# Performance work log

Hardware: AMD Instinct MI355X
Metric: run time of the kernel (lower is better)

The kernel has to match this reference:

```python
import jax, jax.numpy as jnp
import numpy as np

SEQ, B, D = 2048, 16, 1024  # seq_len, batch, input/hidden size

def setup_inputs() -> dict:
    key = jax.random.key(0)
    k1, k2, k3 = jax.random.split(key, 3)
    X = jax.random.normal(k1, (SEQ, B, D), dtype=jnp.float32)
    hidden = jnp.zeros((B, D), dtype=jnp.float32)  # initial hidden state C_0
    # nn.Linear(window*input_size, 3*hidden_size): weight (3D, D), bias (3D,)
    W = jax.random.normal(k2, (3 * D, D), dtype=jnp.float32) / np.float32(np.sqrt(D))
    b = jax.random.normal(k3, (3 * D,), dtype=jnp.float32) * 0.01
    return {"X": X, "hidden": hidden, "W": W, "b": b}

def _forget_mult(F, Z, h0):
    # C_t = F_t * Z_t + (1 - F_t) * C_{t-1}, scanned over seq dim
    def step(h, fz):
        f, z = fz
        h = f * z + (1.0 - f) * h
        return h, h
    _, C = jax.lax.scan(step, h0, (F, Z))
    return C  # (S, B, D)

def reference(X, hidden, W, b):
    # window=1 -> source = X; gate projection
    Y = jnp.einsum('sbd,hd->sbh', X, W) + b        # (S, B, 3D)
    Z, F, O = jnp.split(Y, 3, axis=2)
    Z = jnp.tanh(Z)
    F = jax.nn.sigmoid(F)
    C = _forget_mult(F, Z, hidden)                 # (S, B, D)
    H = jax.nn.sigmoid(O) * C                      # output gate (QRNN-fo)
    return H, C[-1:]                               # (S,B,D), (1,B,D)
```

## Files before the change

kernel.cpp:

```cpp
#include <hip/hip_runtime.h>


#define S_LEN 2048
#define BATCH 16
#define DHID 1024
#define N3 3072
#define MROWS (S_LEN * BATCH)
#define XELEMS ((size_t)MROWS * DHID)
#define WELEMS ((size_t)N3 * DHID)
#define YELEMS ((size_t)MROWS * N3)

typedef __attribute__((ext_vector_type(8))) short bf16x8;
typedef __attribute__((ext_vector_type(4))) float floatx4;
typedef __attribute__((ext_vector_type(4))) unsigned short u16x4;

__device__ __forceinline__ float b2f(unsigned short u) {
  return __uint_as_float(((unsigned)u) << 16);
}
__device__ __forceinline__ unsigned short f2b(float x) {
  unsigned u = __float_as_uint(x);
  u += 0x7fffu + ((u >> 16) & 1u);
  return (unsigned short)(u >> 16);
}
__device__ __forceinline__ float sigmoid_f(float x) {
  return __builtin_amdgcn_rcpf(1.0f + __expf(-x));
}
__device__ __forceinline__ float tanh_f(float x) {
  return 2.0f * __builtin_amdgcn_rcpf(1.0f + __expf(-2.0f * x)) - 1.0f;
}

__device__ __forceinline__ void load_lds16(const unsigned short* g, unsigned short* l) {
  __builtin_amdgcn_global_load_lds(
      (const __attribute__((address_space(1))) void*)g,
      (__attribute__((address_space(3))) void*)l,
      16, 0, 0);
}

__global__ __launch_bounds__(256) void cvt_f32_bf16(
    const float* __restrict__ src, unsigned short* __restrict__ dst, int n4) {
  int i = blockIdx.x * 256 + threadIdx.x;
  if (i < n4) {
    float4 v = ((const float4*)src)[i];
    u16x4 o;
    o.x = f2b(v.x); o.y = f2b(v.y); o.z = f2b(v.z); o.w = f2b(v.w);
    ((u16x4*)dst)[i] = o;
  }
}

__global__ __launch_bounds__(256) void qrnn_gemm(
    const unsigned short* __restrict__ X,
    const unsigned short* __restrict__ W,
    const float* __restrict__ bias,
    unsigned short* __restrict__ Y)
{
  __shared__ __align__(16) unsigned short sA[128 * 64];
  __shared__ __align__(16) unsigned short sB[128 * 64];

  const int tid = threadIdx.x;
  const int w  = tid >> 6;
  const int l  = tid & 63;
  const int lr = l & 15;
  const int lq = l >> 4;
  const int n0B = blockIdx.x * 128;
  const int m0B = blockIdx.y * 128;
  const int wm = (w >> 1) * 64;
  const int wn = (w & 1) * 64;

  floatx4 acc[4][4] = {};

  const unsigned short* gA = X + (size_t)m0B * DHID;
  const unsigned short* gB = W + (size_t)n0B * DHID;
  const int srow = tid >> 3;
  const int scol = (tid & 7) << 3;

  for (int k0 = 0; k0 < DHID; k0 += 64) {
#pragma unroll
    for (int j = 0; j < 4; ++j) {
      load_lds16(gA + (size_t)(j * 32 + srow) * DHID + (k0 + scol),
                 sA + (j * 2048 + w * 512));
      load_lds16(gB + (size_t)(j * 32 + srow) * DHID + (k0 + scol),
                 sB + (j * 2048 + w * 512));
    }
    __syncthreads();

#pragma unroll
    for (int kk = 0; kk < 64; kk += 32) {
      bf16x8 af[4], bf[4];
#pragma unroll
      for (int i = 0; i < 4; ++i) {
        af[i] = *(const bf16x8*)&sA[(wm + i * 16 + lr) * 64 + kk + lq * 8];
      }
#pragma unroll
      for (int j = 0; j < 4; ++j) {
        bf[j] = *(const bf16x8*)&sB[(wn + j * 16 + lr) * 64 + kk + lq * 8];
      }
#pragma unroll
      for (int i = 0; i < 4; ++i) {
#pragma unroll
        for (int j = 0; j < 4; ++j) {
          acc[i][j] = __builtin_amdgcn_mfma_f32_16x16x32_bf16(
              af[i], bf[j], acc[i][j], 0, 0, 0);
        }
      }
    }
    __syncthreads();
  }

  const int seg = n0B >> 10;
#pragma unroll
  for (int j = 0; j < 4; ++j) {
    const int n = n0B + wn + j * 16 + lr;
    const float bv = bias[n];
#pragma unroll
    for (int i = 0; i < 4; ++i) {
      const int mb = m0B + wm + i * 16 + lq * 4;
#pragma unroll
      for (int r = 0; r < 4; ++r) {
        float v = acc[i][j][r] + bv;
        v = (seg == 0) ? tanh_f(v) : sigmoid_f(v);
        Y[(size_t)(mb + r) * N3 + n] = f2b(v);
      }
    }
  }
}

#define U 8
#define NCH (S_LEN / U)
#define SSTRIDE (BATCH * N3)
#define HSTRIDE (BATCH * DHID)

__global__ __launch_bounds__(64) void qrnn_scan(
    const unsigned short* __restrict__ Y,
    const float* __restrict__ h0,
    float* __restrict__ out)
{
  const int t = blockIdx.x * 64 + threadIdx.x;
  const int b = t >> 10;
  const int d = t & 1023;
  const unsigned short* base = Y + (size_t)b * N3 + d;
  float* ho = out + (size_t)b * DHID + d;
  float c = h0[t];

  unsigned short z0[U], f0[U], o0[U], z1[U], f1[U], o1[U];

#define LOADCH(ch, zz, ff, oo) { \
    const unsigned short* p = base + (size_t)(ch) * ((size_t)U * SSTRIDE); \
    _Pragma("unroll") \
    for (int j2 = 0; j2 < U; ++j2) { \
      zz[j2] = p[(size_t)j2 * SSTRIDE]; \
      ff[j2] = p[(size_t)j2 * SSTRIDE + DHID]; \
      oo[j2] = p[(size_t)j2 * SSTRIDE + 2 * DHID]; \
    } }

#define COMPCH(ch, zz, ff, oo) { \
    float* q = ho + (size_t)(ch) * ((size_t)U * HSTRIDE); \
    _Pragma("unroll") \
    for (int j2 = 0; j2 < U; ++j2) { \
      float zv = b2f(zz[j2]); \
      float fv = b2f(ff[j2]); \
      float ov = b2f(oo[j2]); \
      c = fmaf(fv, zv - c, c); \
      q[(size_t)j2 * HSTRIDE] = ov * c; \
    } }

  LOADCH(0, z0, f0, o0);
  for (int ch = 0; ch < NCH; ch += 2) {
    LOADCH(ch + 1, z1, f1, o1);
    COMPCH(ch, z0, f0, o0);
    if (ch + 2 < NCH) LOADCH(ch + 2, z0, f0, o0);
    COMPCH(ch + 1, z1, f1, o1);
  }
  out[(size_t)S_LEN * HSTRIDE + t] = c;
}

extern "C" void kernel_launch(void* const* d_in, const int* in_sizes, int n_in,
                              void* d_out, int out_size, void* d_ws, size_t ws_size,
                              hipStream_t stream) {
  const float* X    = (const float*)d_in[0];
  const float* h0   = (const float*)d_in[1];
  const float* W    = (const float*)d_in[2];
  const float* bias = (const float*)d_in[3];
  float* out = (float*)d_out;

  unsigned short* Ybf = (unsigned short*)d_ws;
  unsigned short* Wbf = Ybf + YELEMS;
  unsigned short* Xbf = (unsigned short*)out;

  cvt_f32_bf16<<<(int)(XELEMS / 4 + 255) / 256, 256, 0, stream>>>(X, Xbf, (int)(XELEMS / 4));
  cvt_f32_bf16<<<(int)(WELEMS / 4 + 255) / 256, 256, 0, stream>>>(W, Wbf, (int)(WELEMS / 4));
  qrnn_gemm<<<dim3(N3 / 128, MROWS / 128), 256, 0, stream>>>(Xbf, Wbf, bias, Ybf);
  qrnn_scan<<<dim3((BATCH * DHID) / 64), 64, 0, stream>>>(Ybf, h0, out);
}
```

Baseline: 676.0 us.

## Parallelize forget-mult scan over sequence chunks with two-pass affine combine

Replaces the single sequential scan, which had only 16K threads walking all 2048 steps, with a chunked parallel scan. Pass 1 computes each chunk's affine transform (A, B) from the Z and F gates. A small combine kernel then propagates the carry across 16 chunks, and pass 2 recomputes the outputs per chunk starting from its carry-in. This adds 16x more parallelism to a latency-bound scan. In exchange, Z and F are read twice, two launches are added, and the converted W buffer is reused as workspace after the GEMM.

```diff
diff --git a/kernel.cpp b/kernel.cpp
--- a/kernel.cpp
+++ b/kernel.cpp
@@ -125,31 +125,98 @@
 }
 
 #define U 8
-#define NCH (S_LEN / U)
+#define PCH 16
+#define LCH (S_LEN / PCH)
+#define SUBCH (LCH / U)
 #define SSTRIDE (BATCH * N3)
 #define HSTRIDE (BATCH * DHID)
-
-__global__ __launch_bounds__(64) void qrnn_scan(
+#define NT (BATCH * DHID)
+
+__global__ __launch_bounds__(256) void qrnn_scan_pass1(
     const unsigned short* __restrict__ Y,
-    const float* __restrict__ h0,
-    float* __restrict__ out)
-{
-  const int t = blockIdx.x * 64 + threadIdx.x;
+    float* __restrict__ Aarr,
+    float* __restrict__ Barr)
+{
+  const int g = blockIdx.x * 256 + threadIdx.x;
+  const int t = g & (NT - 1);
+  const int p = g >> 14;
   const int b = t >> 10;
   const int d = t & 1023;
-  const unsigned short* base = Y + (size_t)b * N3 + d;
-  float* ho = out + (size_t)b * DHID + d;
+  const unsigned short* base =
+      Y + (size_t)(p * LCH) * SSTRIDE + (size_t)b * N3 + d;
+
+  float a = 1.0f, bv = 0.0f;
+  unsigned short z0[U], f0[U], z1[U], f1[U];
+
+#define LOADZF(ch, zz, ff) { \
+    const unsigned short* p_ = base + (size_t)(ch) * ((size_t)U * SSTRIDE); \
+    _Pragma("unroll") \
+    for (int j2 = 0; j2 < U; ++j2) { \
+      zz[j2] = p_[(size_t)j2 * SSTRIDE]; \
+      ff[j2] = p_[(size_t)j2 * SSTRIDE + DHID]; \
+    } }
+
+#define COMPAB(zz, ff) { \
+    _Pragma("unroll") \
+    for (int j2 = 0; j2 < U; ++j2) { \
+      float zv = b2f(zz[j2]); \
+      float fv = b2f(ff[j2]); \
+      a  = fmaf(-fv, a, a);             \
+      bv = fmaf(fv, zv - bv, bv);       \
+    } }
+
+  LOADZF(0, z0, f0);
+  for (int ch = 0; ch < SUBCH; ch += 2) {
+    LOADZF(ch + 1, z1, f1);
+    COMPAB(z0, f0);
+    if (ch + 2 < SUBCH) LOADZF(ch + 2, z0, f0);
+    COMPAB(z1, f1);
+  }
+  Aarr[g] = a;
+  Barr[g] = bv;
+}
+
+__global__ __launch_bounds__(256) void qrnn_combine(
+    const float* __restrict__ Aarr,
+    const float* __restrict__ Barr,
+    const float* __restrict__ h0,
+    float* __restrict__ Cin,
+    float* __restrict__ out)
+{
+  const int t = blockIdx.x * 256 + threadIdx.x;
   float c = h0[t];
+#pragma unroll
+  for (int p = 0; p < PCH; ++p) {
+    Cin[p * NT + t] = c;
+    c = fmaf(Aarr[p * NT + t], c, Barr[p * NT + t]);
+  }
+  out[(size_t)S_LEN * HSTRIDE + t] = c;
+}
+
+__global__ __launch_bounds__(256) void qrnn_scan_pass2(
+    const unsigned short* __restrict__ Y,
+    const float* __restrict__ Cin,
+    float* __restrict__ out)
+{
+  const int g = blockIdx.x * 256 + threadIdx.x;
+  const int t = g & (NT - 1);
+  const int p = g >> 14;
+  const int b = t >> 10;
+  const int d = t & 1023;
+  const unsigned short* base =
+      Y + (size_t)(p * LCH) * SSTRIDE + (size_t)b * N3 + d;
+  float* ho = out + (size_t)(p * LCH) * HSTRIDE + (size_t)b * DHID + d;
+  float c = Cin[g];
 
   unsigned short z0[U], f0[U], o0[U], z1[U], f1[U], o1[U];
 
 #define LOADCH(ch, zz, ff, oo) { \
-    const unsigned short* p = base + (size_t)(ch) * ((size_t)U * SSTRIDE); \
-    _Pragma("unroll") \
-    for (int j2 = 0; j2 < U; ++j2) { \
-      zz[j2] = p[(size_t)j2 * SSTRIDE]; \
-      ff[j2] = p[(size_t)j2 * SSTRIDE + DHID]; \
-      oo[j2] = p[(size_t)j2 * SSTRIDE + 2 * DHID]; \
+    const unsigned short* p_ = base + (size_t)(ch) * ((size_t)U * SSTRIDE); \
+    _Pragma("unroll") \
+    for (int j2 = 0; j2 < U; ++j2) { \
+      zz[j2] = p_[(size_t)j2 * SSTRIDE]; \
+      ff[j2] = p_[(size_t)j2 * SSTRIDE + DHID]; \
+      oo[j2] = p_[(size_t)j2 * SSTRIDE + 2 * DHID]; \
     } }
 
 #define COMPCH(ch, zz, ff, oo) { \
@@ -164,13 +231,12 @@
     } }
 
   LOADCH(0, z0, f0, o0);
-  for (int ch = 0; ch < NCH; ch += 2) {
+  for (int ch = 0; ch < SUBCH; ch += 2) {
     LOADCH(ch + 1, z1, f1, o1);
     COMPCH(ch, z0, f0, o0);
-    if (ch + 2 < NCH) LOADCH(ch + 2, z0, f0, o0);
+    if (ch + 2 < SUBCH) LOADCH(ch + 2, z0, f0, o0);
     COMPCH(ch + 1, z1, f1, o1);
   }
-  out[(size_t)S_LEN * HSTRIDE + t] = c;
 }
 
 extern "C" void kernel_launch(void* const* d_in, const int* in_sizes, int n_in,
@@ -185,9 +251,14 @@
   unsigned short* Ybf = (unsigned short*)d_ws;
   unsigned short* Wbf = Ybf + YELEMS;
   unsigned short* Xbf = (unsigned short*)out;
+  float* Aarr = (float*)Wbf;
+  float* Barr = Aarr + PCH * NT;
+  float* CinA = Barr + PCH * NT;
 
   cvt_f32_bf16<<<(int)(XELEMS / 4 + 255) / 256, 256, 0, stream>>>(X, Xbf, (int)(XELEMS / 4));
   cvt_f32_bf16<<<(int)(WELEMS / 4 + 255) / 256, 256, 0, stream>>>(W, Wbf, (int)(WELEMS / 4));
   qrnn_gemm<<<dim3(N3 / 128, MROWS / 128), 256, 0, stream>>>(Xbf, Wbf, bias, Ybf);
-  qrnn_scan<<<dim3((BATCH * DHID) / 64), 64, 0, stream>>>(Ybf, h0, out);
-}
+  qrnn_scan_pass1<<<dim3((PCH * NT) / 256), 256, 0, stream>>>(Ybf, Aarr, Barr);
+  qrnn_combine<<<dim3(NT / 256), 256, 0, stream>>>(Aarr, Barr, h0, CinA, out);
+  qrnn_scan_pass2<<<dim3((PCH * NT) / 256), 256, 0, stream>>>(Ybf, CinA, out);
+}
```

Measured after the change: 563.5 us. 16.6% less time.
